# Optimization experiments

Measured on AMD Instinct MI355X. Metric: run time of the kernel, lower is better.

The kernel has to match this reference:

```python
import jax, jax.numpy as jnp
from jax import lax
import numpy as np

# 6D tensors: (N, C, h1, w1, h2, w2); weights: (Cout, Cin, k,k,k,k)
DN = lax.ConvDimensionNumbers(lhs_spec=(0, 1, 2, 3, 4, 5),
                              rhs_spec=(0, 1, 2, 3, 4, 5),
                              out_spec=(0, 1, 2, 3, 4, 5))


def conv4d_relu(x, w, b):
    # true 4D convolution, stride 1, SAME padding, then bias + ReLU
    y = lax.conv_general_dilated(x, w, window_strides=(1, 1, 1, 1),
                                 padding='SAME', dimension_numbers=DN)
    return jax.nn.relu(y + b.reshape(1, -1, 1, 1, 1, 1))


def _perm(x):
    # swap the two (h, w) spatial pairs of the correlation tensor
    return jnp.transpose(x, (0, 1, 4, 5, 2, 3))


def _sym(x, w, b):
    # symmetric_mode branch: f(x) + perm(f(perm(x)))
    return conv4d_relu(x, w, b) + _perm(conv4d_relu(_perm(x), w, b))


def setup_inputs() -> dict:
    key = jax.random.key(0)
    ks = jax.random.split(key, 9)
    B, S = 4, 20
    sc = 0.05
    return {
        'x':    jax.random.normal(ks[0], (B, 1, S, S, S, S), dtype=jnp.float32),
        'w0':   jax.random.normal(ks[1], (16, 1, 5, 5, 5, 5), dtype=jnp.float32) * sc,
        'b0':   jax.random.normal(ks[2], (16,), dtype=jnp.float32) * sc,
        'w10':  jax.random.normal(ks[3], (8, 16, 3, 3, 5, 5), dtype=jnp.float32) * sc,
        'b10':  jax.random.normal(ks[4], (8,), dtype=jnp.float32) * sc,
        'w11':  jax.random.normal(ks[5], (8, 16, 5, 5, 5, 5), dtype=jnp.float32) * sc,
        'b11':  jax.random.normal(ks[6], (8,), dtype=jnp.float32) * sc,
        'w2':   jax.random.normal(ks[7], (1, 16, 5, 5, 5, 5), dtype=jnp.float32) * sc,
        'b2':   jax.random.normal(ks[8], (1,), dtype=jnp.float32) * sc,
    }


def reference(x, w0, b0, w10, b10, w11, b11, w2, b2):
    x = _sym(x, w0, b0)                       # [B,16,S,S,S,S]
    x0 = _sym(x, w10, b10)                    # [B, 8,S,S,S,S]
    x1 = _sym(x, w11, b11)                    # [B, 8,S,S,S,S]
    x = jnp.concatenate((x0, x1), axis=1)     # [B,16,S,S,S,S]
    return _sym(x, w2, b2)                    # [B, 1,S,S,S,S]
```

## Files before the change

### kernel.cpp

```cpp
#include <hip/hip_runtime.h>

#define TS 20
#define TS2 400

typedef __attribute__((ext_vector_type(8))) __bf16 bf16x8;
typedef __attribute__((ext_vector_type(4))) __bf16 bf16x4;
typedef __attribute__((ext_vector_type(4))) float  f32x4;
typedef __attribute__((ext_vector_type(4))) int    int4v;

__device__ __forceinline__ float relu_f(float v) { return v > 0.0f ? v : 0.0f; }

#define MFMA16(a, b, c) __builtin_amdgcn_mfma_f32_16x16x32_bf16((a), (b), (c), 0, 0, 0)

#define LPAD 580

__global__ __launch_bounds__(256)
void pack_w0(const float* __restrict__ w0, __bf16* __restrict__ wpk0)
{
    int idx = blockIdx.x * 256 + (int)threadIdx.x;
    if (idx >= 25 * 32 * 32) return;
    const int c = idx & 31;
    const int m = (idx >> 5) & 31;
    const int e = idx >> 10;
    float v = 0.0f;
    if (c < 25) {
        const int co = m & 15;
        const int k1o = c / 5, k2o = c % 5, k3i = e / 5, k4i = e % 5;
        if (m < 16) v = w0[co * 625 + k1o * 125 + k2o * 25 + k3i * 5 + k4i];
        else        v = w0[co * 625 + k3i * 125 + k4i * 25 + k1o * 5 + k2o];
    }
    wpk0[idx] = (__bf16)v;
}

__global__ __launch_bounds__(256)
void pack_wmid(const float* __restrict__ w10, const float* __restrict__ w11,
               __bf16* __restrict__ wpk)
{
    int idx = blockIdx.x * 256 + (int)threadIdx.x;
    if (idx >= 650 * 512) return;
    const int ci  = idx & 15;
    const int m   = (idx >> 4) & 31;
    const int off = idx >> 9;
    const int inner = off % 26, outer = off / 26;
    const int d1 = outer / 5 - 2, d2 = outer % 5 - 2;
    float v = 0.0f;
    if (inner < 25) {
        const int d3 = inner / 5 - 2, d4 = inner % 5 - 2;
        const int co = m & 7;
        const bool isB  = (m & 8)  != 0;
        const bool is11 = (m & 16) != 0;
        if (is11) {
            int k1, k2, k3, k4;
            if (!isB) { k1 = d1 + 2; k2 = d2 + 2; k3 = d3 + 2; k4 = d4 + 2; }
            else      { k1 = d3 + 2; k2 = d4 + 2; k3 = d1 + 2; k4 = d2 + 2; }
            v = w11[((((co * 16 + ci) * 5 + k1) * 5 + k2) * 5 + k3) * 5 + k4];
        } else {
            if (!isB) {
                if (d1 >= -1 && d1 <= 1 && d2 >= -1 && d2 <= 1)
                    v = w10[((((co * 16 + ci) * 3 + (d1 + 1)) * 3 + (d2 + 1)) * 5 + (d3 + 2)) * 5 + (d4 + 2)];
            } else {
                if (d3 >= -1 && d3 <= 1 && d4 >= -1 && d4 <= 1)
                    v = w10[((((co * 16 + ci) * 3 + (d3 + 1)) * 3 + (d4 + 1)) * 5 + (d1 + 2)) * 5 + (d2 + 2)];
            }
        }
    }
    wpk[idx] = (__bf16)v;
}

__global__ __launch_bounds__(256)
void pack_w2f(const float* __restrict__ w2, __bf16* __restrict__ wpk2f)
{
    int idx = blockIdx.x * 256 + (int)threadIdx.x;
    if (idx >= 26 * 64 * 16) return;
    const int ci = idx & 15;
    const int m  = (idx >> 4) & 63;
    const int e  = idx >> 10;
    float v = 0.0f;
    if (e < 25) {
        if (m < 25)
            v = w2[ci * 625 + (m / 5) * 125 + (m % 5) * 25 + (e / 5) * 5 + (e % 5)];
        else if (m >= 32 && m < 57) {
            const int dd = m - 32;
            v = w2[ci * 625 + (e / 5) * 125 + (e % 5) * 25 + (dd / 5) * 5 + (dd % 5)];
        }
    }
    wpk2f[idx] = (__bf16)v;
}

__global__ __launch_bounds__(320)
void conv0_mfma(const float* __restrict__ x, const __bf16* __restrict__ wpk0,
                const float* __restrict__ b0, __bf16* __restrict__ y1)
{
    __shared__ __bf16 lds0[4 * LPAD * 8];

    const int tid  = (int)threadIdx.x;
    const int lane = tid & 63;
    const int wave = tid >> 6;
    const int bid  = blockIdx.x;
    const int o2 = bid % TS, o1 = (bid / TS) % TS, n = bid / TS2;

    for (int i = tid; i < 4 * LPAD * 8 / 2; i += 320) ((int*)lds0)[i] = 0;
    __syncthreads();

    for (int c = tid; c < 25 * TS2; c += 320) {
        const int pl = c / TS2, pt = c % TS2;
        const int i1 = o1 + pl / 5 - 2, i2 = o2 + pl % 5 - 2;
        if (i1 >= 0 && i1 < TS && i2 >= 0 && i2 < TS) {
            const float v = x[(size_t)((n * TS + i1) * TS + i2) * TS2 + pt];
            const int L = (pt / TS + 2) * 24 + (pt % TS + 2);
            lds0[((pl >> 3) * LPAD + L) * 8 + (pl & 7)] = (__bf16)v;
        }
    }
    __syncthreads();

    const int mrow = lane & 15;
    const int sub  = lane >> 4;

    int sb[5];
#pragma unroll
    for (int i = 0; i < 5; ++i) {
        const int p = (wave * 5 + i) * 16 + mrow;
        sb[i] = (sub * LPAD + (p / TS + 2) * 24 + (p % TS + 2)) * 8;
    }

    f32x4 acc0[5], acc1[5];
#pragma unroll
    for (int i = 0; i < 5; ++i) {
        acc0[i] = (f32x4){0.f, 0.f, 0.f, 0.f};
        acc1[i] = (f32x4){0.f, 0.f, 0.f, 0.f};
    }

    bf16x8 a0 = *(const bf16x8*)(wpk0 + (size_t)mrow * 32 + sub * 8);
    bf16x8 a1 = *(const bf16x8*)(wpk0 + (size_t)(16 + mrow) * 32 + sub * 8);
    for (int e = 0; e < 25; ++e) {
        bf16x8 na0 = a0, na1 = a1;
        if (e < 24) {
            na0 = *(const bf16x8*)(wpk0 + ((size_t)((e + 1) * 32 + mrow)) * 32 + sub * 8);
            na1 = *(const bf16x8*)(wpk0 + ((size_t)((e + 1) * 32 + 16 + mrow)) * 32 + sub * 8);
        }
        const int delta = ((e / 5 - 2) * 24 + (e % 5 - 2)) * 8;
#pragma unroll
        for (int i = 0; i < 5; ++i) {
            bf16x8 bfr = *(const bf16x8*)(&lds0[sb[i] + delta]);
            acc0[i] = MFMA16(a0, bfr, acc0[i]);
            acc1[i] = MFMA16(a1, bfr, acc1[i]);
        }
        a0 = na0; a1 = na1;
    }

    const f32x4 bv = *(const f32x4*)(b0 + sub * 4);
#pragma unroll
    for (int i = 0; i < 5; ++i) {
        const int p = (wave * 5 + i) * 16 + mrow;
        bf16x4 pk;
#pragma unroll
        for (int r = 0; r < 4; ++r)
            pk[r] = (__bf16)(relu_f(acc0[i][r] + bv[r]) + relu_f(acc1[i][r] + bv[r]));
        *(bf16x4*)(y1 + ((size_t)bid * TS2 + p) * 16 + sub * 4) = pk;
    }
}

__global__ __launch_bounds__(320)
void conv4d_mid_mfma(const __bf16* __restrict__ y1, const __bf16* __restrict__ wpk,
                     const float* __restrict__ b10, const float* __restrict__ b11,
                     __bf16* __restrict__ y2)
{
    __shared__ __bf16 lds[2][9216];

    const int tid  = (int)threadIdx.x;
    const int lane = tid & 63;
    const int wave = tid >> 6;
    const int bid0 = blockIdx.x;
    const int bid  = (bid0 & 7) * 200 + (bid0 >> 3);
    const int o2 = bid % TS, o1 = (bid / TS) % TS, n = bid / TS2;

    for (int i = tid; i < 9216; i += 320) ((int*)lds)[i] = 0;

    const int mrow = lane & 15;
    const int sub  = lane >> 4;
    const int ci0  = (sub & 1) * 8;
    const int aoff = (sub >> 1) * 512 + mrow * 16 + ci0;

    int sbase[5];
#pragma unroll
    for (int i = 0; i < 5; ++i) {
        const int p  = (wave * 5 + i) * 16 + mrow;
        sbase[i] = ((p / TS + 2) * 24 + (p % TS + 2)) * 16 + ci0;
    }

    f32x4 acc[5][2];
#pragma unroll
    for (int i = 0; i < 5; ++i) {
        acc[i][0] = (f32x4){0.f, 0.f, 0.f, 0.f};
        acc[i][1] = (f32x4){0.f, 0.f, 0.f, 0.f};
    }

    __syncthreads();

    int buf = 0;
    for (int d1 = -2; d1 <= 2; ++d1) {
        const int i1 = o1 + d1;
        if (i1 < 0 || i1 >= TS) continue;
        for (int d2 = -2; d2 <= 2; ++d2) {
            const int i2 = o2 + d2;
            if (i2 < 0 || i2 >= TS) continue;

            const __bf16* src = y1 + (size_t)((n * TS + i1) * TS + i2) * TS2 * 16;
            for (int c = tid; c < 800; c += 320) {
                const int h = c / 40, rem = c % 40;
                int4v v = *(const int4v*)(src + c * 8);
                *(int4v*)(&lds[buf][((h + 2) * 24 + 2) * 16 + rem * 8]) = v;
            }
            __syncthreads();

            const int outer = (d1 + 2) * 5 + (d2 + 2);
            const __bf16* wbase = wpk + (size_t)outer * 26 * 512;

            bf16x8 a0 = *(const bf16x8*)(wbase + aoff);
            bf16x8 a1 = *(const bf16x8*)(wbase + aoff + 256);
            for (int ic = 0; ic < 13; ++ic) {
                bf16x8 na0 = a0, na1 = a1;
                if (ic < 12) {
                    na0 = *(const bf16x8*)(wbase + (ic + 1) * 1024 + aoff);
                    na1 = *(const bf16x8*)(wbase + (ic + 1) * 1024 + aoff + 256);
                }
                const int e = 2 * ic + (sub >> 1);
                int d3 = 0, d4 = 0;
                if (e < 25) { d3 = e / 5 - 2; d4 = e % 5 - 2; }
                const int delta = (d3 * 24 + d4) * 16;
#pragma unroll
                for (int i = 0; i < 5; ++i) {
                    bf16x8 bfr = *(const bf16x8*)(&lds[buf][sbase[i] + delta]);
                    acc[i][0] = MFMA16(a0, bfr, acc[i][0]);
                    acc[i][1] = MFMA16(a1, bfr, acc[i][1]);
                }
                a0 = na0; a1 = na1;
            }
            buf ^= 1;
        }
    }

    const size_t base = (size_t)bid * TS2 * 16;
#pragma unroll
    for (int i = 0; i < 5; ++i) {
        const int p = (wave * 5 + i) * 16 + mrow;
#pragma unroll
        for (int mt = 0; mt < 2; ++mt) {
            const float* bs = mt ? b11 : b10;
            const f32x4 bv = *(const f32x4*)(bs + (sub & 1) * 4);
            bf16x4 pk;
#pragma unroll
            for (int r = 0; r < 4; ++r) {
                float v = relu_f(acc[i][mt][r] + bv[r]);
                float o = v + __shfl_xor(v, 32);
                pk[r] = (__bf16)o;
            }
            if (lane < 32)
                *(bf16x4*)(y2 + base + (size_t)p * 16 + mt * 8 + (sub & 1) * 4) = pk;
        }
    }
}

__global__ __launch_bounds__(320)
void conv2t_mfma(const __bf16* __restrict__ y2, const __bf16* __restrict__ wpk2f,
                 int n0, __bf16* __restrict__ t)
{
    __shared__ __bf16 lds[2 * LPAD * 8];

    const int tid  = (int)threadIdx.x;
    const int lane = tid & 63;
    const int wave = tid >> 6;
    const int bid = blockIdx.x;
    const int q2 = bid % TS, q1 = (bid / TS) % TS, nl = bid / TS2;

    for (int i = tid; i < 2 * LPAD * 8 / 2; i += 320) ((int*)lds)[i] = 0;
    __syncthreads();

    const __bf16* src = y2 + (size_t)(((n0 + nl) * TS + q1) * TS + q2) * TS2 * 16;
    for (int c = tid; c < 800; c += 320) {
        const int h = c / 40, rem = c % 40;
        const int w = rem >> 1, cb = rem & 1;
        int4v v = *(const int4v*)(src + c * 8);
        *(int4v*)(&lds[(cb * LPAD + (h + 2) * 24 + 2 + w) * 8]) = v;
    }
    __syncthreads();

    const int mrow = lane & 15;
    const int sub  = lane >> 4;

    int sbase[5];
#pragma unroll
    for (int i = 0; i < 5; ++i) {
        const int p  = (wave * 5 + i) * 16 + mrow;
        sbase[i] = ((sub & 1) * LPAD + (p / TS + 2) * 24 + (p % TS + 2)) * 8;
    }

    f32x4 acc[5][4];
#pragma unroll
    for (int i = 0; i < 5; ++i)
#pragma unroll
        for (int mt = 0; mt < 4; ++mt)
            acc[i][mt] = (f32x4){0.f, 0.f, 0.f, 0.f};

    for (int ic = 0; ic < 13; ++ic) {
        const int e = 2 * ic + (sub >> 1);
        int d3 = 0, d4 = 0;
        if (e < 25) { d3 = e / 5 - 2; d4 = e % 5 - 2; }
        const int delta = (d3 * 24 + d4) * 8;
        const __bf16* abase = wpk2f + ((size_t)e * 64 + mrow) * 16 + (sub & 1) * 8;
        bf16x8 a0 = *(const bf16x8*)(abase);
        bf16x8 a1 = *(const bf16x8*)(abase + 256);
        bf16x8 a2 = *(const bf16x8*)(abase + 512);
        bf16x8 a3 = *(const bf16x8*)(abase + 768);
#pragma unroll
        for (int i = 0; i < 5; ++i) {
            bf16x8 bfr = *(const bf16x8*)(&lds[sbase[i] + delta]);
            acc[i][0] = MFMA16(a0, bfr, acc[i][0]);
            acc[i][1] = MFMA16(a1, bfr, acc[i][1]);
            acc[i][2] = MFMA16(a2, bfr, acc[i][2]);
            acc[i][3] = MFMA16(a3, bfr, acc[i][3]);
        }
    }

    __bf16* tb = t + (size_t)((nl * TS + q1) * TS + q2) * (50 * TS2);
#pragma unroll
    for (int i = 0; i < 5; ++i) {
        const int p = (wave * 5 + i) * 16 + mrow;
#pragma unroll
        for (int mt = 0; mt < 4; ++mt) {
#pragma unroll
            for (int r = 0; r < 4; ++r) {
                const int gm = mt * 16 + sub * 4 + r;
                int m50 = -1;
                if (gm < 25) m50 = gm;
                else if (gm >= 32 && gm < 57) m50 = gm - 7;
                if (m50 >= 0) tb[m50 * TS2 + p] = (__bf16)acc[i][mt][r];
            }
        }
    }
}

__global__ __launch_bounds__(448)
void conv2_sum(const __bf16* __restrict__ t, const float* __restrict__ b2,
               int n0, float* __restrict__ out)
{
    const int tid = (int)threadIdx.x;
    if (tid >= TS2) return;
    const int bid = blockIdx.x;
    const int o2 = bid % TS, o1 = (bid / TS) % TS, nl = bid / TS2;

    float accA = 0.0f, accB = 0.0f;
    for (int dd = 0; dd < 25; ++dd) {
        const int q1 = o1 + dd / 5 - 2, q2 = o2 + dd % 5 - 2;
        if (q1 < 0 || q1 >= TS || q2 < 0 || q2 >= TS) continue;
        const __bf16* tb = t + (size_t)((nl * TS + q1) * TS + q2) * (50 * TS2) + tid;
        accA += (float)tb[dd * TS2];
        accB += (float)tb[(25 + dd) * TS2];
    }
    const float bias = b2[0];
    out[(size_t)(n0 + nl) * (TS2 * (size_t)TS2) + (size_t)(o1 * TS + o2) * TS2 + tid] =
        relu_f(accA + bias) + relu_f(accB + bias);
}

extern "C" void kernel_launch(void* const* d_in, const int* in_sizes, int n_in,
                              void* d_out, int out_size, void* d_ws, size_t ws_size,
                              hipStream_t stream)
{
    const float* x   = (const float*)d_in[0];
    const float* w0  = (const float*)d_in[1];
    const float* b0  = (const float*)d_in[2];
    const float* w10 = (const float*)d_in[3];
    const float* b10 = (const float*)d_in[4];
    const float* w11 = (const float*)d_in[5];
    const float* b11 = (const float*)d_in[6];
    const float* w2  = (const float*)d_in[7];
    const float* b2  = (const float*)d_in[8];
    float* out = (float*)d_out;

    __bf16* y1    = (__bf16*)d_ws;
    __bf16* y2    = y1 + (size_t)10240000;
    __bf16* tbuf  = y2 + (size_t)10240000;
    __bf16* wpkm  = tbuf + (size_t)16000000;
    __bf16* wpk0  = wpkm + 650 * 512;
    __bf16* wpk2f = wpk0 + 25 * 32 * 32;

    dim3 blk320(320), blk256(256), blk448(448);

    pack_w0  <<<dim3((25600 + 255) / 256),  blk256, 0, stream>>>(w0, wpk0);
    pack_wmid<<<dim3((332800 + 255) / 256), blk256, 0, stream>>>(w10, w11, wpkm);
    pack_w2f <<<dim3((26624 + 255) / 256),  blk256, 0, stream>>>(w2, wpk2f);

    conv0_mfma     <<<dim3(4 * TS * TS), blk320, 0, stream>>>(x, wpk0, b0, y1);
    conv4d_mid_mfma<<<dim3(1600),        blk320, 0, stream>>>(y1, wpkm, b10, b11, y2);

    for (int n0 = 0; n0 < 4; n0 += 2) {
        conv2t_mfma<<<dim3(800), blk320, 0, stream>>>(y2, wpk2f, n0, tbuf);
        conv2_sum  <<<dim3(800), blk448, 0, stream>>>(tbuf, b2, n0, out);
    }
}
```

Measured before the change: 483.6 us.

## Prefetch next input slab into registers to overlap global loads with MFMA

Restructures the layer-1 kernel's outer loop so the global loads of the next valid (i1,i2) input slab are issued into registers before the MFMA compute on the current LDS buffer, then written to the alternate LDS buffer at the start of the next iteration. This hides global-memory latency behind the matrix work instead of stalling on load-then-sync. It also raises wave priority with s_setprio during the MFMA loop and precomputes the LDS write offsets. The cost is extra live registers for the staged data, which may affect occupancy.

New measurement: 495.7 us. 2.5% more time.

```diff
diff --git a/kernel.cpp b/kernel.cpp
--- a/kernel.cpp
+++ b/kernel.cpp
@@ -181,6 +181,12 @@
     const int ci0  = (sub & 1) * 8;
     const int aoff = (sub >> 1) * 512 + mrow * 16 + ci0;
 
+    const int wo0 = ((tid / 40 + 2) * 24 + 2) * 16 + (tid % 40) * 8;
+    const int wo1 = (((tid + 320) / 40 + 2) * 24 + 2) * 16 + ((tid + 320) % 40) * 8;
+    const int wo2 = (((tid + 640) / 40 + 2) * 24 + 2) * 16 + ((tid + 640) % 40) * 8;
+    const bool c2ok = tid < 160;
+    const __bf16* ybase = y1 + (size_t)n * TS2 * TS2 * 16;
+
     int sbase[5];
 #pragma unroll
     for (int i = 0; i < 5; ++i) {
@@ -195,49 +201,71 @@
         acc[i][1] = (f32x4){0.f, 0.f, 0.f, 0.f};
     }
 
+    int kk = 0;
+    {
+        while (kk < 25) {
+            const int i1 = o1 + kk / 5 - 2, i2 = o2 + kk % 5 - 2;
+            if (i1 >= 0 && i1 < TS && i2 >= 0 && i2 < TS) break;
+            ++kk;
+        }
+    }
+    int4v s0, s1, s2;
+    {
+        const int i1 = o1 + kk / 5 - 2, i2 = o2 + kk % 5 - 2;
+        const __bf16* src = ybase + (size_t)(i1 * TS + i2) * TS2 * 16;
+        s0 = *(const int4v*)(src + tid * 8);
+        s1 = *(const int4v*)(src + (tid + 320) * 8);
+        if (c2ok) s2 = *(const int4v*)(src + (tid + 640) * 8);
+    }
     __syncthreads();
 
     int buf = 0;
-    for (int d1 = -2; d1 <= 2; ++d1) {
-        const int i1 = o1 + d1;
-        if (i1 < 0 || i1 >= TS) continue;
-        for (int d2 = -2; d2 <= 2; ++d2) {
-            const int i2 = o2 + d2;
-            if (i2 < 0 || i2 >= TS) continue;
-
-            const __bf16* src = y1 + (size_t)((n * TS + i1) * TS + i2) * TS2 * 16;
-            for (int c = tid; c < 800; c += 320) {
-                const int h = c / 40, rem = c % 40;
-                int4v v = *(const int4v*)(src + c * 8);
-                *(int4v*)(&lds[buf][((h + 2) * 24 + 2) * 16 + rem * 8]) = v;
+    while (kk < 25) {
+        *(int4v*)(&lds[buf][wo0]) = s0;
+        *(int4v*)(&lds[buf][wo1]) = s1;
+        if (c2ok) *(int4v*)(&lds[buf][wo2]) = s2;
+        __syncthreads();
+
+        int nk = kk + 1;
+        while (nk < 25) {
+            const int i1 = o1 + nk / 5 - 2, i2 = o2 + nk % 5 - 2;
+            if (i1 >= 0 && i1 < TS && i2 >= 0 && i2 < TS) break;
+            ++nk;
+        }
+        if (nk < 25) {
+            const int i1 = o1 + nk / 5 - 2, i2 = o2 + nk % 5 - 2;
+            const __bf16* src = ybase + (size_t)(i1 * TS + i2) * TS2 * 16;
+            s0 = *(const int4v*)(src + tid * 8);
+            s1 = *(const int4v*)(src + (tid + 320) * 8);
+            if (c2ok) s2 = *(const int4v*)(src + (tid + 640) * 8);
+        }
+
+        const __bf16* wbase = wpk + (size_t)kk * 26 * 512;
+        bf16x8 a0 = *(const bf16x8*)(wbase + aoff);
+        bf16x8 a1 = *(const bf16x8*)(wbase + aoff + 256);
+        __builtin_amdgcn_s_setprio(1);
+        for (int ic = 0; ic < 13; ++ic) {
+            bf16x8 na0 = a0, na1 = a1;
+            if (ic < 12) {
+                na0 = *(const bf16x8*)(wbase + (ic + 1) * 1024 + aoff);
+                na1 = *(const bf16x8*)(wbase + (ic + 1) * 1024 + aoff + 256);
             }
-            __syncthreads();
-
-            const int outer = (d1 + 2) * 5 + (d2 + 2);
-            const __bf16* wbase = wpk + (size_t)outer * 26 * 512;
-
-            bf16x8 a0 = *(const bf16x8*)(wbase + aoff);
-            bf16x8 a1 = *(const bf16x8*)(wbase + aoff + 256);
-            for (int ic = 0; ic < 13; ++ic) {
-                bf16x8 na0 = a0, na1 = a1;
-                if (ic < 12) {
-                    na0 = *(const bf16x8*)(wbase + (ic + 1) * 1024 + aoff);
-                    na1 = *(const bf16x8*)(wbase + (ic + 1) * 1024 + aoff + 256);
-                }
-                const int e = 2 * ic + (sub >> 1);
-                int d3 = 0, d4 = 0;
-                if (e < 25) { d3 = e / 5 - 2; d4 = e % 5 - 2; }
-                const int delta = (d3 * 24 + d4) * 16;
-#pragma unroll
-                for (int i = 0; i < 5; ++i) {
-                    bf16x8 bfr = *(const bf16x8*)(&lds[buf][sbase[i] + delta]);
-                    acc[i][0] = MFMA16(a0, bfr, acc[i][0]);
-                    acc[i][1] = MFMA16(a1, bfr, acc[i][1]);
-                }
-                a0 = na0; a1 = na1;
+            const int e = 2 * ic + (sub >> 1);
+            int d3 = 0, d4 = 0;
+            if (e < 25) { d3 = e / 5 - 2; d4 = e % 5 - 2; }
+            const int delta = (d3 * 24 + d4) * 16;
+#pragma unroll
+            for (int i = 0; i < 5; ++i) {
+                bf16x8 bfr = *(const bf16x8*)(&lds[buf][sbase[i] + delta]);
+                acc[i][0] = MFMA16(a0, bfr, acc[i][0]);
+                acc[i][1] = MFMA16(a1, bfr, acc[i][1]);
             }
-            buf ^= 1;
-        }
+            a0 = na0; a1 = na1;
+        }
+        __builtin_amdgcn_s_setprio(0);
+
+        buf ^= 1;
+        kk = nk;
     }
 
     const size_t base = (size_t)bid * TS2 * 16;
```
